# Kernel tuning notes

Hardware: AMD Instinct MI355X
Metric: run time of the kernel (lower is better)

## Reference

```python
import jax, jax.numpy as jnp
import numpy as np

NUM_NODES = 100_000
NUM_EDGES = 1_200_000
NUM_REL = 3
EMBED_DIM = 64
HIDDEN_DIM = 64
NUM_CLS = 2
NUM_GRAPHS = 512


def setup_inputs() -> dict:
    key = jax.random.key(0)
    ks = jax.random.split(key, 12)
    s = 1.0 / np.sqrt(EMBED_DIM)
    inp = {
        # forward args
        "x": jnp.zeros((NUM_NODES,), dtype=jnp.int64),  # vocab size 1 -> all zeros
        "edge_index": jax.random.randint(ks[0], (2, NUM_EDGES), 0, NUM_NODES, dtype=jnp.int64),
        "edge_type": jax.random.randint(ks[1], (NUM_EDGES,), 0, NUM_REL, dtype=jnp.int64),
        "batch": jnp.sort(jax.random.randint(ks[2], (NUM_NODES,), 0, NUM_GRAPHS, dtype=jnp.int64)),
        # parameters
        "embed_w": jax.random.normal(ks[3], (1, EMBED_DIM), jnp.float32),
        "W1": jax.random.normal(ks[4], (NUM_REL, EMBED_DIM, HIDDEN_DIM), jnp.float32) * s,
        "root1": jax.random.normal(ks[5], (EMBED_DIM, HIDDEN_DIM), jnp.float32) * s,
        "b1": jnp.zeros((HIDDEN_DIM,), jnp.float32),
        "W2": jax.random.normal(ks[6], (NUM_REL, HIDDEN_DIM, HIDDEN_DIM), jnp.float32) * s,
        "root2": jax.random.normal(ks[7], (HIDDEN_DIM, HIDDEN_DIM), jnp.float32) * s,
        "b2": jnp.zeros((HIDDEN_DIM,), jnp.float32),
        "lin_w": jax.random.normal(ks[8], (HIDDEN_DIM, NUM_CLS), jnp.float32) * s,
        "lin_b": jnp.zeros((NUM_CLS,), jnp.float32),
    }
    return inp


def rgcn_conv(h, W, root, b, src, dst, edge_type):
    """PyG RGCNConv with mean aggregation per relation + root weight + bias."""
    n = h.shape[0]
    out = h @ root + b  # root/self contribution, [N, H]
    for r in range(NUM_REL):
        m = (edge_type == r).astype(h.dtype)  # [E]
        tr = h @ W[r]                          # [N, H] small GEMM
        msg = tr[src] * m[:, None]             # gather [E, H]
        ssum = jax.ops.segment_sum(msg, dst, num_segments=n)  # scatter-add [N, H]
        cnt = jax.ops.segment_sum(m, dst, num_segments=n)     # per-relation in-degree
        out = out + ssum / jnp.clip(cnt, 1.0)[:, None]        # mean aggregation
    return out


def reference(x, edge_index, edge_type, batch, embed_w, W1, root1, b1, W2, root2, b2, lin_w, lin_b):
    src, dst = edge_index[0], edge_index[1]
    h = embed_w[x]                                       # [N, D] embedding lookup
    h = jax.nn.relu(rgcn_conv(h, W1, root1, b1, src, dst, edge_type))
    h = jax.nn.relu(rgcn_conv(h, W2, root2, b2, src, dst, edge_type))
    # global mean pool over graphs
    gsum = jax.ops.segment_sum(h, batch, num_segments=NUM_GRAPHS)            # [G, H]
    gcnt = jax.ops.segment_sum(jnp.ones_like(h[:, 0]), batch, num_segments=NUM_GRAPHS)
    g_emb = gsum / jnp.clip(gcnt, 1.0)[:, None]
    return g_emb @ lin_w + lin_b                          # [G, num_cls]
```

## Files before the change

### kernel.cpp

```cpp
#include <hip/hip_runtime.h>

#define NODES   100000
#define EDGES   1200000
#define NREL    3
#define DIM     64
#define NGRAPH  512

#define BSH     8
#define NB      391
#define BUCKCAP 4096
#define SBLK    256
#define CHUNK   4688
#define MBPITCH 100352

#define OFF_GSUM  0
#define OFF_GCNT  131072
#define OFF_CUR   133120
#define OFF_MB    135168
#define OFF_ZEND  436224
#define OFF_REC   436224
#define OFF_BASE  6842368
#define OFF_T2    6844416

__global__ void k_tab(const float* __restrict__ embed_w, const float* __restrict__ W1,
                      const float* __restrict__ root1, const float* __restrict__ b1,
                      const float* __restrict__ W2, const float* __restrict__ root2,
                      const float* __restrict__ b2,
                      float* __restrict__ base, float* __restrict__ T2,
                      char* __restrict__ ws) {
    {
        uint4* z = (uint4*)ws;
        const uint4 zz = make_uint4(0, 0, 0, 0);
        const int gt = blockIdx.x * 256 + threadIdx.x;
        for (int i = gt; i < OFF_ZEND / 16; i += 32 * 256) z[i] = zz;
    }
    __shared__ float h0[DIM];
    __shared__ float u[DIM];
    __shared__ float t[NREL][DIM];
    __shared__ float h1s[8][DIM];
    __shared__ float red[4][DIM];
    const int tid = threadIdx.x;
    const int j = tid & 63, w = tid >> 6;
    if (tid < DIM) h0[tid] = embed_w[tid];
    __syncthreads();
    {
        const float* M = (w == 0) ? root1 : (W1 + (size_t)(w - 1) * DIM * DIM);
        float s = 0.f;
        for (int k = 0; k < DIM; ++k) s += h0[k] * M[k * DIM + j];
        if (w == 0) u[j] = s + b1[j];
        else        t[w - 1][j] = s;
    }
    __syncthreads();
    for (int p = w; p < 8; p += 4) {
        float v = u[j];
        if (p & 1) v += t[0][j];
        if (p & 2) v += t[1][j];
        if (p & 4) v += t[2][j];
        h1s[p][j] = fmaxf(v, 0.f);
    }
    __syncthreads();
    const int row = blockIdx.x;
    const int p = (row < 8) ? row : ((row - 8) & 7);
    const float* M = (row < 8) ? root2 : (W2 + (size_t)((row - 8) >> 3) * DIM * DIM);
    float s = 0.f;
    for (int k = w * 16; k < w * 16 + 16; ++k) s += h1s[p][k] * M[k * DIM + j];
    red[w][j] = s;
    __syncthreads();
    if (w == 0) {
        const float v = red[0][j] + red[1][j] + red[2][j] + red[3][j];
        if (row < 8) base[p * DIM + j] = v + b2[j];
        else         T2[(row - 8) * DIM + j] = v;
    }
}

__global__ void k_scat(const int* __restrict__ ei, const int* __restrict__ et,
                       int* __restrict__ cursor, unsigned int* __restrict__ rec,
                       unsigned char* __restrict__ mb) {
    __shared__ int hist[NB];
    __shared__ int cur[NB];
    const int tid = threadIdx.x;
    for (int b = tid; b < NB; b += 256) hist[b] = 0;
    __syncthreads();
    const int e0 = blockIdx.x * CHUNK;
    const int* src = ei;
    const int* dst = ei + EDGES;
    for (int i = tid; i < CHUNK / 4; i += 256) {
        const int e = e0 + i * 4;
        if (e < EDGES) {
            const int4 d4 = *(const int4*)(dst + e);
            atomicAdd(&hist[d4.x >> BSH], 1);
            atomicAdd(&hist[d4.y >> BSH], 1);
            atomicAdd(&hist[d4.z >> BSH], 1);
            atomicAdd(&hist[d4.w >> BSH], 1);
        }
    }
    __syncthreads();
    for (int b = tid; b < NB; b += 256) {
        const int h = hist[b];
        const int r = h ? atomicAdd(&cursor[b], h) : 0;
        cur[b] = b * BUCKCAP + r;
    }
    __syncthreads();
    for (int i = tid; i < CHUNK / 4; i += 256) {
        const int e = e0 + i * 4;
        if (e < EDGES) {
            const int4 s4 = *(const int4*)(src + e);
            const int4 d4 = *(const int4*)(dst + e);
            const int4 r4 = *(const int4*)(et + e);
            int p;
            p = atomicAdd(&cur[d4.x >> BSH], 1);
            if (p < ((d4.x >> BSH) + 1) * BUCKCAP)
                rec[p] = ((unsigned)(d4.x & 255) << 19) | ((unsigned)r4.x << 17) | (unsigned)s4.x;
            mb[r4.x * MBPITCH + d4.x] = 1;
            p = atomicAdd(&cur[d4.y >> BSH], 1);
            if (p < ((d4.y >> BSH) + 1) * BUCKCAP)
                rec[p] = ((unsigned)(d4.y & 255) << 19) | ((unsigned)r4.y << 17) | (unsigned)s4.y;
            mb[r4.y * MBPITCH + d4.y] = 1;
            p = atomicAdd(&cur[d4.z >> BSH], 1);
            if (p < ((d4.z >> BSH) + 1) * BUCKCAP)
                rec[p] = ((unsigned)(d4.z & 255) << 19) | ((unsigned)r4.z << 17) | (unsigned)s4.z;
            mb[r4.z * MBPITCH + d4.z] = 1;
            p = atomicAdd(&cur[d4.w >> BSH], 1);
            if (p < ((d4.w >> BSH) + 1) * BUCKCAP)
                rec[p] = ((unsigned)(d4.w & 255) << 19) | ((unsigned)r4.w << 17) | (unsigned)s4.w;
            mb[r4.w * MBPITCH + d4.w] = 1;
        }
    }
}

__global__ void k_histnode(const unsigned int* __restrict__ rec,
                           const int* __restrict__ cursor,
                           const unsigned char* __restrict__ mb,
                           const int* __restrict__ batch,
                           const float* __restrict__ base, const float* __restrict__ T2,
                           float* __restrict__ gsum, int* __restrict__ gcnt) {
    __shared__ unsigned int h[3072];
    __shared__ float bs[8 * DIM];
    __shared__ float ts[24 * DIM];
    const int tid = threadIdx.x;
    for (int i = tid; i < 3072; i += 512) h[i] = 0;
    for (int i = tid; i < 8 * DIM; i += 512) bs[i] = base[i];
    for (int i = tid; i < 24 * DIM; i += 512) ts[i] = T2[i];
    __syncthreads();
    const int b = blockIdx.x;
    const int s = b * BUCKCAP;
    int n = cursor[b];
    if (n > BUCKCAP) n = BUCKCAP;
    for (int i = tid; i < n; i += 512) {
        const unsigned r32 = rec[s + i];
        const int sv = r32 & 0x1FFFF;
        const int p = mb[sv] | (mb[MBPITCH + sv] << 1) | (mb[2 * MBPITCH + sv] << 2);
        const int idx = (r32 >> 19) * 24 + ((r32 >> 17) & 3) * 8 + p;
        atomicAdd(&h[idx >> 1], 1u << ((idx & 1) * 16));
    }
    __syncthreads();
    const int lane = tid & 63;
    const int w = tid >> 6;
    const int v0 = (b << BSH) + w * 32;
    float acc = 0.f;
    int curg = -1, runlen = 0;
    for (int i = 0; i < 32; ++i) {
        const int v = v0 + i;
        if (v >= NODES) break;
        const int pm = mb[v] | (mb[MBPITCH + v] << 1) | (mb[2 * MBPITCH + v] << 2);
        float sacc = bs[pm * DIM + lane];
        const unsigned* hv = &h[(v & 255) * 12];
        for (int r = 0; r < NREL; ++r) {
            float msg = 0.f;
            int cr = 0;
            #pragma unroll
            for (int q = 0; q < 4; ++q) {
                const unsigned x = hv[r * 4 + q];
                const int c0 = (int)(x & 0xFFFFu), c1 = (int)(x >> 16);
                cr += c0 + c1;
                msg += (float)c0 * ts[(r * 8 + 2 * q) * DIM + lane]
                     + (float)c1 * ts[(r * 8 + 2 * q + 1) * DIM + lane];
            }
            sacc += msg / fmaxf((float)cr, 1.0f);
        }
        sacc = fmaxf(sacc, 0.f);
        const int g = batch[v];
        if (g != curg) {
            if (curg >= 0) {
                atomicAdd(&gsum[curg * DIM + lane], acc);
                if (lane == 0) atomicAdd(&gcnt[curg], runlen);
            }
            curg = g; acc = 0.f; runlen = 0;
        }
        acc += sacc; runlen++;
    }
    if (curg >= 0) {
        atomicAdd(&gsum[curg * DIM + lane], acc);
        if (lane == 0) atomicAdd(&gcnt[curg], runlen);
    }
}

__global__ void k_final(const float* __restrict__ gsum, const int* __restrict__ gcnt,
                        const float* __restrict__ lin_w, const float* __restrict__ lin_b,
                        float* __restrict__ out) {
    const int lane = threadIdx.x & 63;
    const int g = blockIdx.x * (blockDim.x >> 6) + (threadIdx.x >> 6);
    if (g >= NGRAPH) return;
    const float inv = 1.0f / fmaxf((float)gcnt[g], 1.0f);
    const float s = gsum[g * DIM + lane] * inv;
    float p0 = s * lin_w[lane * 2 + 0];
    float p1 = s * lin_w[lane * 2 + 1];
    for (int off = 32; off; off >>= 1) {
        p0 += __shfl_down(p0, off);
        p1 += __shfl_down(p1, off);
    }
    if (lane == 0) {
        out[g * 2 + 0] = p0 + lin_b[0];
        out[g * 2 + 1] = p1 + lin_b[1];
    }
}

extern "C" void kernel_launch(void* const* d_in, const int* in_sizes, int n_in,
                              void* d_out, int out_size, void* d_ws, size_t ws_size,
                              hipStream_t stream) {
    const int*   ei      = (const int*)d_in[1];
    const int*   et      = (const int*)d_in[2];
    const int*   batch   = (const int*)d_in[3];
    const float* embed_w = (const float*)d_in[4];
    const float* W1      = (const float*)d_in[5];
    const float* root1   = (const float*)d_in[6];
    const float* b1      = (const float*)d_in[7];
    const float* W2      = (const float*)d_in[8];
    const float* root2   = (const float*)d_in[9];
    const float* b2      = (const float*)d_in[10];
    const float* lin_w   = (const float*)d_in[11];
    const float* lin_b   = (const float*)d_in[12];
    float* out = (float*)d_out;

    char* ws = (char*)d_ws;
    float*         gsum = (float*)(ws + OFF_GSUM);
    int*           gcnt = (int*)(ws + OFF_GCNT);
    int*           cur  = (int*)(ws + OFF_CUR);
    unsigned char* mb   = (unsigned char*)(ws + OFF_MB);
    unsigned int*  rec  = (unsigned int*)(ws + OFF_REC);
    float*         base = (float*)(ws + OFF_BASE);
    float*         T2   = (float*)(ws + OFF_T2);

    k_tab     <<<32,   256, 0, stream>>>(embed_w, W1, root1, b1, W2, root2, b2,
                                         base, T2, ws);
    k_scat    <<<SBLK, 256, 0, stream>>>(ei, et, cur, rec, mb);
    k_histnode<<<NB,   512, 0, stream>>>(rec, cur, mb, batch, base, T2, gsum, gcnt);
    k_final   <<<128,  256, 0, stream>>>(gsum, gcnt, lin_w, lin_b, out);
}
```

Baseline: 163.3 us.

## Interleave per-relation masks per node, widen histnode blocks, shuffle batch/mask loads

The three per-relation byte masks move from a planar layout to an interleaved 4-bytes-per-node layout, so each source lookup in the histogram phase becomes a single 32-bit load instead of three scattered byte loads. The node-aggregation kernel goes to 1024 threads, each wave now covering 16 nodes. Batch ids and masks are preloaded once per wave and broadcast with shuffles, and relation groups with zero counts are skipped. The zeroed workspace region grows, and the scatter writes one byte at a stride of 4 per edge, which may add some contention.

Result: faster. 143.6 us (-12.1%).

```diff
diff --git a/kernel.cpp b/kernel.cpp
--- a/kernel.cpp
+++ b/kernel.cpp
@@ -11,16 +11,15 @@
 #define BUCKCAP 4096
 #define SBLK    256
 #define CHUNK   4688
-#define MBPITCH 100352
 
 #define OFF_GSUM  0
 #define OFF_GCNT  131072
 #define OFF_CUR   133120
-#define OFF_MB    135168
-#define OFF_ZEND  436224
-#define OFF_REC   436224
-#define OFF_BASE  6842368
-#define OFF_T2    6844416
+#define OFF_MBN   135168
+#define OFF_ZEND  535552
+#define OFF_REC   535552
+#define OFF_BASE  6941696
+#define OFF_T2    6943744
 
 __global__ void k_tab(const float* __restrict__ embed_w, const float* __restrict__ W1,
                       const float* __restrict__ root1, const float* __restrict__ b1,
@@ -75,7 +74,7 @@
 
 __global__ void k_scat(const int* __restrict__ ei, const int* __restrict__ et,
                        int* __restrict__ cursor, unsigned int* __restrict__ rec,
-                       unsigned char* __restrict__ mb) {
+                       unsigned char* __restrict__ mbn) {
     __shared__ int hist[NB];
     __shared__ int cur[NB];
     const int tid = threadIdx.x;
@@ -111,26 +110,26 @@
             p = atomicAdd(&cur[d4.x >> BSH], 1);
             if (p < ((d4.x >> BSH) + 1) * BUCKCAP)
                 rec[p] = ((unsigned)(d4.x & 255) << 19) | ((unsigned)r4.x << 17) | (unsigned)s4.x;
-            mb[r4.x * MBPITCH + d4.x] = 1;
+            mbn[d4.x * 4 + r4.x] = 1;
             p = atomicAdd(&cur[d4.y >> BSH], 1);
             if (p < ((d4.y >> BSH) + 1) * BUCKCAP)
                 rec[p] = ((unsigned)(d4.y & 255) << 19) | ((unsigned)r4.y << 17) | (unsigned)s4.y;
-            mb[r4.y * MBPITCH + d4.y] = 1;
+            mbn[d4.y * 4 + r4.y] = 1;
             p = atomicAdd(&cur[d4.z >> BSH], 1);
             if (p < ((d4.z >> BSH) + 1) * BUCKCAP)
                 rec[p] = ((unsigned)(d4.z & 255) << 19) | ((unsigned)r4.z << 17) | (unsigned)s4.z;
-            mb[r4.z * MBPITCH + d4.z] = 1;
+            mbn[d4.z * 4 + r4.z] = 1;
             p = atomicAdd(&cur[d4.w >> BSH], 1);
             if (p < ((d4.w >> BSH) + 1) * BUCKCAP)
                 rec[p] = ((unsigned)(d4.w & 255) << 19) | ((unsigned)r4.w << 17) | (unsigned)s4.w;
-            mb[r4.w * MBPITCH + d4.w] = 1;
+            mbn[d4.w * 4 + r4.w] = 1;
         }
     }
 }
 
 __global__ void k_histnode(const unsigned int* __restrict__ rec,
                            const int* __restrict__ cursor,
-                           const unsigned char* __restrict__ mb,
+                           const unsigned char* __restrict__ mbn,
                            const int* __restrict__ batch,
                            const float* __restrict__ base, const float* __restrict__ T2,
                            float* __restrict__ gsum, int* __restrict__ gcnt) {
@@ -138,48 +137,62 @@
     __shared__ float bs[8 * DIM];
     __shared__ float ts[24 * DIM];
     const int tid = threadIdx.x;
-    for (int i = tid; i < 3072; i += 512) h[i] = 0;
-    for (int i = tid; i < 8 * DIM; i += 512) bs[i] = base[i];
-    for (int i = tid; i < 24 * DIM; i += 512) ts[i] = T2[i];
+    const unsigned* mbn32 = (const unsigned*)mbn;
+    for (int i = tid; i < 3072; i += 1024) h[i] = 0;
+    for (int i = tid; i < 8 * DIM; i += 1024) bs[i] = base[i];
+    for (int i = tid; i < 24 * DIM; i += 1024) ts[i] = T2[i];
     __syncthreads();
     const int b = blockIdx.x;
     const int s = b * BUCKCAP;
     int n = cursor[b];
     if (n > BUCKCAP) n = BUCKCAP;
-    for (int i = tid; i < n; i += 512) {
+    for (int i = tid; i < n; i += 1024) {
         const unsigned r32 = rec[s + i];
-        const int sv = r32 & 0x1FFFF;
-        const int p = mb[sv] | (mb[MBPITCH + sv] << 1) | (mb[2 * MBPITCH + sv] << 2);
+        const unsigned x = mbn32[r32 & 0x1FFFF];
+        const int p = (x & 1) | ((x >> 7) & 2) | ((x >> 14) & 4);
         const int idx = (r32 >> 19) * 24 + ((r32 >> 17) & 3) * 8 + p;
         atomicAdd(&h[idx >> 1], 1u << ((idx & 1) * 16));
     }
     __syncthreads();
     const int lane = tid & 63;
     const int w = tid >> 6;
-    const int v0 = (b << BSH) + w * 32;
+    const int v0 = (b << BSH) + w * 16;
+    if (v0 >= NODES) return;
+    int pidx = v0 + (lane & 15);
+    if (pidx >= NODES) pidx = NODES - 1;
+    const int bv = batch[pidx];
+    const int mv = (int)mbn32[pidx];
     float acc = 0.f;
     int curg = -1, runlen = 0;
-    for (int i = 0; i < 32; ++i) {
+    for (int i = 0; i < 16; ++i) {
         const int v = v0 + i;
         if (v >= NODES) break;
-        const int pm = mb[v] | (mb[MBPITCH + v] << 1) | (mb[2 * MBPITCH + v] << 2);
+        const int mx = __shfl(mv, i);
+        const int pm = (mx & 1) | ((mx >> 7) & 2) | ((mx >> 14) & 4);
         float sacc = bs[pm * DIM + lane];
         const unsigned* hv = &h[(v & 255) * 12];
+        #pragma unroll
         for (int r = 0; r < NREL; ++r) {
-            float msg = 0.f;
-            int cr = 0;
-            #pragma unroll
-            for (int q = 0; q < 4; ++q) {
-                const unsigned x = hv[r * 4 + q];
-                const int c0 = (int)(x & 0xFFFFu), c1 = (int)(x >> 16);
-                cr += c0 + c1;
-                msg += (float)c0 * ts[(r * 8 + 2 * q) * DIM + lane]
-                     + (float)c1 * ts[(r * 8 + 2 * q + 1) * DIM + lane];
+            const unsigned x0 = hv[r * 4 + 0], x1 = hv[r * 4 + 1];
+            const unsigned x2 = hv[r * 4 + 2], x3 = hv[r * 4 + 3];
+            const int cr = (int)((x0 & 0xFFFF) + (x0 >> 16) + (x1 & 0xFFFF) + (x1 >> 16)
+                               + (x2 & 0xFFFF) + (x2 >> 16) + (x3 & 0xFFFF) + (x3 >> 16));
+            if (cr > 0) {
+                float msg = 0.f;
+                const float* tr = &ts[r * 8 * DIM + lane];
+                if (x0) msg += (float)(x0 & 0xFFFF) * tr[0 * DIM]
+                             + (float)(x0 >> 16)    * tr[1 * DIM];
+                if (x1) msg += (float)(x1 & 0xFFFF) * tr[2 * DIM]
+                             + (float)(x1 >> 16)    * tr[3 * DIM];
+                if (x2) msg += (float)(x2 & 0xFFFF) * tr[4 * DIM]
+                             + (float)(x2 >> 16)    * tr[5 * DIM];
+                if (x3) msg += (float)(x3 & 0xFFFF) * tr[6 * DIM]
+                             + (float)(x3 >> 16)    * tr[7 * DIM];
+                sacc += msg / (float)cr;
             }
-            sacc += msg / fmaxf((float)cr, 1.0f);
         }
         sacc = fmaxf(sacc, 0.f);
-        const int g = batch[v];
+        const int g = __shfl(bv, i);
         if (g != curg) {
             if (curg >= 0) {
                 atomicAdd(&gsum[curg * DIM + lane], acc);
@@ -236,14 +249,14 @@
     float*         gsum = (float*)(ws + OFF_GSUM);
     int*           gcnt = (int*)(ws + OFF_GCNT);
     int*           cur  = (int*)(ws + OFF_CUR);
-    unsigned char* mb   = (unsigned char*)(ws + OFF_MB);
+    unsigned char* mbn  = (unsigned char*)(ws + OFF_MBN);
     unsigned int*  rec  = (unsigned int*)(ws + OFF_REC);
     float*         base = (float*)(ws + OFF_BASE);
     float*         T2   = (float*)(ws + OFF_T2);
 
-    k_tab     <<<32,   256, 0, stream>>>(embed_w, W1, root1, b1, W2, root2, b2,
-                                         base, T2, ws);
-    k_scat    <<<SBLK, 256, 0, stream>>>(ei, et, cur, rec, mb);
-    k_histnode<<<NB,   512, 0, stream>>>(rec, cur, mb, batch, base, T2, gsum, gcnt);
-    k_final   <<<128,  256, 0, stream>>>(gsum, gcnt, lin_w, lin_b, out);
-}
+    k_tab     <<<32,   256,  0, stream>>>(embed_w, W1, root1, b1, W2, root2, b2,
+                                          base, T2, ws);
+    k_scat    <<<SBLK, 256,  0, stream>>>(ei, et, cur, rec, mbn);
+    k_histnode<<<NB,   1024, 0, stream>>>(rec, cur, mbn, batch, base, T2, gsum, gcnt);
+    k_final   <<<128,  256,  0, stream>>>(gsum, gcnt, lin_w, lin_b, out);
+}
```
